# Performance work log

Measured on AMD Instinct MI355X. Metric: run time of the kernel, lower is better.

## Reference

```python
import jax, jax.numpy as jnp
import numpy as np

B, L, C, N = 64, 512, 1, 128  # batch, max seq len, num_conjugates, num_tags


def setup_inputs() -> dict:
    key = jax.random.key(0)
    k1, k2, k3, k4, k5 = jax.random.split(key, 5)
    emissions = jax.random.normal(k1, (B, L, C, N), dtype=jnp.float32)
    transitions = jax.random.normal(k2, (C, N, N), dtype=jnp.float32) * 0.01
    start_transitions = jax.random.normal(k3, (C, N), dtype=jnp.float32) * 0.01
    end_transitions = jax.random.normal(k4, (C, N), dtype=jnp.float32) * 0.01
    lengths = jax.random.randint(k5, (B,), 1, L + 1)  # valid lengths in [1, L]
    return {
        "emissions": emissions,
        "transitions": transitions,
        "start_transitions": start_transitions,
        "end_transitions": end_transitions,
        "lengths": lengths,
    }


def reference(emissions, transitions, start_transitions, end_transitions, lengths):
    # CRF log-partition (forward algorithm in the log semiring).
    # emissions: [B, L, C, N]; transitions: [C, N, N]; start/end: [C, N]; lengths: [B]
    b, l, c, n = emissions.shape
    # alpha_0 = start + emission at t=0  -> [B, C, N]
    alpha0 = start_transitions[None, :, :] + emissions[:, 0]

    e_rest = jnp.moveaxis(emissions[:, 1:], 1, 0)  # [L-1, B, C, N]
    t_idx = jnp.arange(1, l)

    def step(alpha, inp):
        e_t, t = inp
        # log-semiring mat-vec: logsumexp over previous tag axis
        scores = alpha[..., :, None] + transitions[None] + e_t[..., None, :]  # [B,C,N,N]
        new_alpha = jax.nn.logsumexp(scores, axis=2)  # [B, C, N]
        active = (t < lengths)[:, None, None]  # ragged mask: freeze finished sequences
        return jnp.where(active, new_alpha, alpha), None

    alpha, _ = jax.lax.scan(step, alpha0, (e_rest, t_idx))
    # terminate with end transitions -> log partition per (batch, conjugate)
    return jax.nn.logsumexp(alpha + end_transitions[None, :, :], axis=-1)  # [B, C]
```

## Files before the change

### kernel.cpp

```cpp
#include <hip/hip_runtime.h>


#define LOG2E 1.4426950408889634f
#define LN2   0.6931471805599453f

#define LDS_BARRIER() asm volatile("s_waitcnt lgkmcnt(0)\n\ts_barrier" ::: "memory")

typedef float    f2 __attribute__((ext_vector_type(2)));
typedef _Float16 h2 __attribute__((ext_vector_type(2)));

#define PKRTZ(a, b) __builtin_bit_cast(h2, __builtin_amdgcn_cvt_pkrtz((a), (b)))

template <int CTRL>
__device__ __forceinline__ float dpp_f(float x) {
    return __int_as_float(
        __builtin_amdgcn_mov_dpp(__float_as_int(x), CTRL, 0xF, 0xF, false));
}

__global__ __launch_bounds__(256)
__attribute__((amdgpu_waves_per_eu(1, 1)))
void crf_halves(
    const float* __restrict__ emissions,
    const float* __restrict__ transitions,
    const float* __restrict__ start_t,
    const float* __restrict__ end_t,
    const int*   __restrict__ lengths,
    float* __restrict__ wsV,
    int*   __restrict__ wsO)
{
    constexpr int N = 128;
    constexpr int L = 512;
    const int  bid = blockIdx.x;
    const bool isf = bid < 64;
    const int  b   = isf ? bid : bid - 64;
    const int  tid = threadIdx.x;
    const int  g   = tid >> 2;
    const int  k   = tid & 3;

    __shared__ alignas(16) float pbuf[2][80];

    h2 EA_0,  EA_1,  EA_2,  EA_3,  EA_4,  EA_5,  EA_6,  EA_7;
    h2 EA_8,  EA_9,  EA_10, EA_11, EA_12, EA_13, EA_14, EA_15;
    h2 EB_0,  EB_1,  EB_2,  EB_3,  EB_4,  EB_5,  EB_6,  EB_7;
    h2 EB_8,  EB_9,  EB_10, EB_11, EB_12, EB_13, EB_14, EB_15;
    if (isf) {
        const float* tb = transitions + (size_t)(32 * k) * N + 2 * g;
#define INIT_F(m)                                                              \
        {                                                                      \
            f2 r0 = *reinterpret_cast<const f2*>(tb + (size_t)(2 * (m)) * N);  \
            f2 r1 = *reinterpret_cast<const f2*>(tb + (size_t)(2 * (m) + 1) * N); \
            EA_##m = PKRTZ(__builtin_amdgcn_exp2f(r0.x * LOG2E),               \
                           __builtin_amdgcn_exp2f(r1.x * LOG2E));              \
            EB_##m = PKRTZ(__builtin_amdgcn_exp2f(r0.y * LOG2E),               \
                           __builtin_amdgcn_exp2f(r1.y * LOG2E));              \
        }
        INIT_F(0)  INIT_F(1)  INIT_F(2)  INIT_F(3)
        INIT_F(4)  INIT_F(5)  INIT_F(6)  INIT_F(7)
        INIT_F(8)  INIT_F(9)  INIT_F(10) INIT_F(11)
        INIT_F(12) INIT_F(13) INIT_F(14) INIT_F(15)
#undef INIT_F
    } else {
        const float* ra_ = transitions + (size_t)(2 * g) * N + 32 * k;
        const float* rb_ = transitions + (size_t)(2 * g + 1) * N + 32 * k;
#define INIT_B(m)                                                              \
        {                                                                      \
            f2 r0 = *reinterpret_cast<const f2*>(ra_ + 2 * (m));               \
            f2 r1 = *reinterpret_cast<const f2*>(rb_ + 2 * (m));               \
            EA_##m = PKRTZ(__builtin_amdgcn_exp2f(r0.x * LOG2E),               \
                           __builtin_amdgcn_exp2f(r0.y * LOG2E));              \
            EB_##m = PKRTZ(__builtin_amdgcn_exp2f(r1.x * LOG2E),               \
                           __builtin_amdgcn_exp2f(r1.y * LOG2E));              \
        }
        INIT_B(0)  INIT_B(1)  INIT_B(2)  INIT_B(3)
        INIT_B(4)  INIT_B(5)  INIT_B(6)  INIT_B(7)
        INIT_B(8)  INIT_B(9)  INIT_B(10) INIT_B(11)
        INIT_B(12) INIT_B(13) INIT_B(14) INIT_B(15)
#undef INIT_B
    }

    const int len = lengths[b];
    const int m   = (len - 1) >> 1;
    const float* eb = emissions + (size_t)b * L * N;

    int n_steps, e0, dstep; bool zfinal;
    if (isf) {
        n_steps = m; e0 = 1; dstep = 1; zfinal = false;
    } else {
        int total = len - 1 - m;
        n_steps = total > 0 ? total - 1 : 0;
        e0 = len - 2; if (e0 < 0) e0 = 0;
        dstep = -1;
        zfinal = total > 0;
    }

    int o = 0, cur = 0;
    float qA, qB;
    {
        const float* base = isf ? start_t : end_t;
        f2 bt = *reinterpret_cast<const f2*>(base + 2 * g);
        f2 ev;
        if (isf)         ev = *reinterpret_cast<const f2*>(eb + 2 * g);
        else if (zfinal) ev = *reinterpret_cast<const f2*>(eb + (size_t)(len - 1) * N + 2 * g);
        else           { ev.x = 0.f; ev.y = 0.f; }
        qA = __builtin_amdgcn_exp2f((bt.x + ev.x) * LOG2E);
        qB = __builtin_amdgcn_exp2f((bt.y + ev.y) * LOG2E);
        if (k == 0)
            pbuf[0][(g >> 4) * 20 + (g & 15)] =
                __builtin_bit_cast(float, PKRTZ(qA, qB));
    }
    LDS_BARRIER();

    auto eidx = [&](int n) {
        int nn = (n < n_steps) ? n : (n_steps - 1);
        if (nn < 0) nn = 0;
        return e0 + dstep * nn;
    };
    auto ldE = [&](int tt) {
        return *reinterpret_cast<const f2*>(eb + (size_t)tt * N + 2 * g);
    };

    auto STEP = [&](f2 ecur) {
        float q0w = pbuf[cur][0];
        const float4* pv = reinterpret_cast<const float4*>(&pbuf[cur][k * 20]);
        float4 Q0 = pv[0], Q1 = pv[1], Q2 = pv[2], Q3 = pv[3];

        unsigned u0 = __float_as_uint(q0w);
        int eS = (int)((u0 >> 10) & 0x1Fu) - 15;
        o += eS;
        float feS = (float)eS;
        float esA = __builtin_amdgcn_exp2f(ecur.x * LOG2E - feS);
        float esB = __builtin_amdgcn_exp2f(ecur.y * LOG2E - feS);

        float aA0 = 0.f, aA1 = 0.f, aB0 = 0.f, aB1 = 0.f;
#define D0(m_, Qc)                                                             \
        {                                                                      \
            h2 pm = __builtin_bit_cast(h2, Qc);                                \
            aA0 = __builtin_amdgcn_fdot2(pm, EA_##m_, aA0, false);             \
            aB0 = __builtin_amdgcn_fdot2(pm, EB_##m_, aB0, false);             \
        }
#define D1(m_, Qc)                                                             \
        {                                                                      \
            h2 pm = __builtin_bit_cast(h2, Qc);                                \
            aA1 = __builtin_amdgcn_fdot2(pm, EA_##m_, aA1, false);             \
            aB1 = __builtin_amdgcn_fdot2(pm, EB_##m_, aB1, false);             \
        }
        D0(0,  Q0.x) D1(1,  Q0.y) D0(2,  Q0.z) D1(3,  Q0.w)
        D0(4,  Q1.x) D1(5,  Q1.y) D0(6,  Q1.z) D1(7,  Q1.w)
        D0(8,  Q2.x) D1(9,  Q2.y) D0(10, Q2.z) D1(11, Q2.w)
        D0(12, Q3.x) D1(13, Q3.y) D0(14, Q3.z) D1(15, Q3.w)
#undef D0
#undef D1
        float dA = aA0 + aA1;
        float dB = aB0 + aB1;

        dA += dpp_f<0xB1>(dA); dB += dpp_f<0xB1>(dB);
        dA += dpp_f<0x4E>(dA); dB += dpp_f<0x4E>(dB);

        qA = esA * dA;
        qB = esB * dB;
        cur ^= 1;
        if (k == 0)
            pbuf[cur][(g >> 4) * 20 + (g & 15)] =
                __builtin_bit_cast(float, PKRTZ(qA, qB));
        LDS_BARRIER();
    };

    f2 ra = ldE(eidx(0));
    f2 rb = ldE(eidx(1));
    f2 rc = ldE(eidx(2));
    f2 rd = ldE(eidx(3));

    int n = 0;
    while (n < n_steps) {
        STEP(ra); ra = ldE(eidx(n + 4)); ++n; if (n >= n_steps) break;
        STEP(rb); rb = ldE(eidx(n + 4)); ++n; if (n >= n_steps) break;
        STEP(rc); rc = ldE(eidx(n + 4)); ++n; if (n >= n_steps) break;
        STEP(rd); rd = ldE(eidx(n + 4)); ++n;
    }
    if (zfinal) {
        f2 z; z.x = 0.f; z.y = 0.f;
        STEP(z);
    }

    float* wv = wsV + (size_t)((isf ? 0 : 64) + b) * 128;
    if (k == 0) {
        f2 q; q.x = qA; q.y = qB;
        *reinterpret_cast<f2*>(wv + 2 * g) = q;
    }
    if (tid == 0) wsO[(isf ? 0 : 64) + b] = o;
}

__global__ __launch_bounds__(64)
void crf_combine(const float* __restrict__ wsV, const int* __restrict__ wsO,
                 const int* __restrict__ lengths, float* __restrict__ out)
{
    const int b = blockIdx.x;
    const int g = threadIdx.x;
    f2 a = *reinterpret_cast<const f2*>(wsV + (size_t)b * 128 + 2 * g);
    f2 x = *reinterpret_cast<const f2*>(wsV + (size_t)(64 + b) * 128 + 2 * g);
    float v = a.x * x.x + a.y * x.y;
    #pragma unroll
    for (int s = 1; s < 64; s <<= 1) v += __shfl_xor(v, s);
    if (g == 0)
        out[b] = LN2 * ((float)(wsO[b] + wsO[64 + b]) +
                        __builtin_amdgcn_logf(v));
}

extern "C" void kernel_launch(void* const* d_in, const int* in_sizes, int n_in,
                              void* d_out, int out_size, void* d_ws, size_t ws_size,
                              hipStream_t stream) {
    const float* emissions   = (const float*)d_in[0];
    const float* transitions = (const float*)d_in[1];
    const float* start_t     = (const float*)d_in[2];
    const float* end_t       = (const float*)d_in[3];
    const int*   lengths     = (const int*)d_in[4];
    float* out = (float*)d_out;

    float* wsV = (float*)d_ws;
    int*   wsO = (int*)((char*)d_ws + 2 * 64 * 128 * sizeof(float));

    crf_halves<<<dim3(128), dim3(256), 0, stream>>>(
        emissions, transitions, start_t, end_t, lengths, wsV, wsO);
    crf_combine<<<dim3(64), dim3(64), 0, stream>>>(wsV, wsO, lengths, out);
}
```

Measured before the change: 131.5 us.

## Split CRF recurrence into four segments using MFMA matrix-product blocks for middle quarters

The sequence is now split into four quarters instead of two halves. The first and last quarters keep the forward and backward vector recurrences. The two middle quarters are computed by new blocks that build transfer-matrix products with 32x32x16 f16 MFMA instructions, using per-wave exponent rescaling. A reworked combine kernel multiplies the forward vector through both fp16 matrices and dots the result with the backward vector. This halves the serial dependency chain per block but adds matrix-matrix work, a 32 KB fp16 matrix write per block, and extra fp16 precision and scaling risk.

```diff
diff --git a/kernel.cpp b/kernel.cpp
--- a/kernel.cpp
+++ b/kernel.cpp
@@ -5,11 +5,17 @@
 #define LN2   0.6931471805599453f
 
 #define LDS_BARRIER() asm volatile("s_waitcnt lgkmcnt(0)\n\ts_barrier" ::: "memory")
-
-typedef float    f2 __attribute__((ext_vector_type(2)));
-typedef _Float16 h2 __attribute__((ext_vector_type(2)));
+#define LGKM0() asm volatile("s_waitcnt lgkmcnt(0)" ::: "memory")
+
+typedef float    f2  __attribute__((ext_vector_type(2)));
+typedef float    f4  __attribute__((ext_vector_type(4)));
+typedef float    f16f __attribute__((ext_vector_type(16)));
+typedef unsigned u4  __attribute__((ext_vector_type(4)));
+typedef _Float16 h2  __attribute__((ext_vector_type(2)));
+typedef _Float16 h8  __attribute__((ext_vector_type(8)));
 
 #define PKRTZ(a, b) __builtin_bit_cast(h2, __builtin_amdgcn_cvt_pkrtz((a), (b)))
+#define BITS(x)     __builtin_bit_cast(unsigned, (x))
 
 template <int CTRL>
 __device__ __forceinline__ float dpp_f(float x) {
@@ -19,191 +25,352 @@
 
 __global__ __launch_bounds__(256)
 __attribute__((amdgpu_waves_per_eu(1, 1)))
-void crf_halves(
+void crf_fused(
     const float* __restrict__ emissions,
     const float* __restrict__ transitions,
     const float* __restrict__ start_t,
     const float* __restrict__ end_t,
     const int*   __restrict__ lengths,
     float* __restrict__ wsV,
-    int*   __restrict__ wsO)
+    int*   __restrict__ wsO,
+    int*   __restrict__ wsMo,
+    _Float16* __restrict__ wsMh)
 {
     constexpr int N = 128;
     constexpr int L = 512;
-    const int  bid = blockIdx.x;
-    const bool isf = bid < 64;
-    const int  b   = isf ? bid : bid - 64;
-    const int  tid = threadIdx.x;
-    const int  g   = tid >> 2;
-    const int  k   = tid & 3;
+    const int bid  = blockIdx.x;
+    const int role = bid >> 6;
+    const int b    = bid & 63;
+    const int tid  = threadIdx.x;
+
+    const int len = lengths[b];
+    const int T   = len - 1;
+    const int qa  = T >> 2;
+    const int qb  = T >> 1;
+    const int qc  = (3 * T) >> 2;
+    const float* eb = emissions + (size_t)b * L * N;
 
     __shared__ alignas(16) float pbuf[2][80];
-
-    h2 EA_0,  EA_1,  EA_2,  EA_3,  EA_4,  EA_5,  EA_6,  EA_7;
-    h2 EA_8,  EA_9,  EA_10, EA_11, EA_12, EA_13, EA_14, EA_15;
-    h2 EB_0,  EB_1,  EB_2,  EB_3,  EB_4,  EB_5,  EB_6,  EB_7;
-    h2 EB_8,  EB_9,  EB_10, EB_11, EB_12, EB_13, EB_14, EB_15;
-    if (isf) {
-        const float* tb = transitions + (size_t)(32 * k) * N + 2 * g;
+    __shared__ alignas(16) float sbuf[4][128];
+
+    if (role < 2) {
+        const bool isf = (role == 0);
+        const int  g   = tid >> 2;
+        const int  k   = tid & 3;
+
+        h2 EA_0,  EA_1,  EA_2,  EA_3,  EA_4,  EA_5,  EA_6,  EA_7;
+        h2 EA_8,  EA_9,  EA_10, EA_11, EA_12, EA_13, EA_14, EA_15;
+        h2 EB_0,  EB_1,  EB_2,  EB_3,  EB_4,  EB_5,  EB_6,  EB_7;
+        h2 EB_8,  EB_9,  EB_10, EB_11, EB_12, EB_13, EB_14, EB_15;
+        if (isf) {
+            const float* tb = transitions + (size_t)(32 * k) * N + 2 * g;
 #define INIT_F(m)                                                              \
-        {                                                                      \
-            f2 r0 = *reinterpret_cast<const f2*>(tb + (size_t)(2 * (m)) * N);  \
-            f2 r1 = *reinterpret_cast<const f2*>(tb + (size_t)(2 * (m) + 1) * N); \
-            EA_##m = PKRTZ(__builtin_amdgcn_exp2f(r0.x * LOG2E),               \
-                           __builtin_amdgcn_exp2f(r1.x * LOG2E));              \
-            EB_##m = PKRTZ(__builtin_amdgcn_exp2f(r0.y * LOG2E),               \
-                           __builtin_amdgcn_exp2f(r1.y * LOG2E));              \
-        }
-        INIT_F(0)  INIT_F(1)  INIT_F(2)  INIT_F(3)
-        INIT_F(4)  INIT_F(5)  INIT_F(6)  INIT_F(7)
-        INIT_F(8)  INIT_F(9)  INIT_F(10) INIT_F(11)
-        INIT_F(12) INIT_F(13) INIT_F(14) INIT_F(15)
+            {                                                                  \
+                f2 r0 = *reinterpret_cast<const f2*>(tb + (size_t)(2 * (m)) * N); \
+                f2 r1 = *reinterpret_cast<const f2*>(tb + (size_t)(2 * (m) + 1) * N); \
+                EA_##m = PKRTZ(__builtin_amdgcn_exp2f(r0.x * LOG2E),           \
+                               __builtin_amdgcn_exp2f(r1.x * LOG2E));          \
+                EB_##m = PKRTZ(__builtin_amdgcn_exp2f(r0.y * LOG2E),           \
+                               __builtin_amdgcn_exp2f(r1.y * LOG2E));          \
+            }
+            INIT_F(0)  INIT_F(1)  INIT_F(2)  INIT_F(3)
+            INIT_F(4)  INIT_F(5)  INIT_F(6)  INIT_F(7)
+            INIT_F(8)  INIT_F(9)  INIT_F(10) INIT_F(11)
+            INIT_F(12) INIT_F(13) INIT_F(14) INIT_F(15)
 #undef INIT_F
-    } else {
-        const float* ra_ = transitions + (size_t)(2 * g) * N + 32 * k;
-        const float* rb_ = transitions + (size_t)(2 * g + 1) * N + 32 * k;
+        } else {
+            const float* ra_ = transitions + (size_t)(2 * g) * N + 32 * k;
+            const float* rb_ = transitions + (size_t)(2 * g + 1) * N + 32 * k;
 #define INIT_B(m)                                                              \
-        {                                                                      \
-            f2 r0 = *reinterpret_cast<const f2*>(ra_ + 2 * (m));               \
-            f2 r1 = *reinterpret_cast<const f2*>(rb_ + 2 * (m));               \
-            EA_##m = PKRTZ(__builtin_amdgcn_exp2f(r0.x * LOG2E),               \
-                           __builtin_amdgcn_exp2f(r0.y * LOG2E));              \
-            EB_##m = PKRTZ(__builtin_amdgcn_exp2f(r1.x * LOG2E),               \
-                           __builtin_amdgcn_exp2f(r1.y * LOG2E));              \
-        }
-        INIT_B(0)  INIT_B(1)  INIT_B(2)  INIT_B(3)
-        INIT_B(4)  INIT_B(5)  INIT_B(6)  INIT_B(7)
-        INIT_B(8)  INIT_B(9)  INIT_B(10) INIT_B(11)
-        INIT_B(12) INIT_B(13) INIT_B(14) INIT_B(15)
+            {                                                                  \
+                f2 r0 = *reinterpret_cast<const f2*>(ra_ + 2 * (m));           \
+                f2 r1 = *reinterpret_cast<const f2*>(rb_ + 2 * (m));           \
+                EA_##m = PKRTZ(__builtin_amdgcn_exp2f(r0.x * LOG2E),           \
+                               __builtin_amdgcn_exp2f(r0.y * LOG2E));          \
+                EB_##m = PKRTZ(__builtin_amdgcn_exp2f(r1.x * LOG2E),           \
+                               __builtin_amdgcn_exp2f(r1.y * LOG2E));          \
+            }
+            INIT_B(0)  INIT_B(1)  INIT_B(2)  INIT_B(3)
+            INIT_B(4)  INIT_B(5)  INIT_B(6)  INIT_B(7)
+            INIT_B(8)  INIT_B(9)  INIT_B(10) INIT_B(11)
+            INIT_B(12) INIT_B(13) INIT_B(14) INIT_B(15)
 #undef INIT_B
-    }
-
-    const int len = lengths[b];
-    const int m   = (len - 1) >> 1;
-    const float* eb = emissions + (size_t)b * L * N;
-
-    int n_steps, e0, dstep; bool zfinal;
-    if (isf) {
-        n_steps = m; e0 = 1; dstep = 1; zfinal = false;
-    } else {
-        int total = len - 1 - m;
-        n_steps = total > 0 ? total - 1 : 0;
-        e0 = len - 2; if (e0 < 0) e0 = 0;
-        dstep = -1;
-        zfinal = total > 0;
-    }
-
-    int o = 0, cur = 0;
-    float qA, qB;
-    {
-        const float* base = isf ? start_t : end_t;
-        f2 bt = *reinterpret_cast<const f2*>(base + 2 * g);
-        f2 ev;
-        if (isf)         ev = *reinterpret_cast<const f2*>(eb + 2 * g);
-        else if (zfinal) ev = *reinterpret_cast<const f2*>(eb + (size_t)(len - 1) * N + 2 * g);
-        else           { ev.x = 0.f; ev.y = 0.f; }
-        qA = __builtin_amdgcn_exp2f((bt.x + ev.x) * LOG2E);
-        qB = __builtin_amdgcn_exp2f((bt.y + ev.y) * LOG2E);
-        if (k == 0)
-            pbuf[0][(g >> 4) * 20 + (g & 15)] =
-                __builtin_bit_cast(float, PKRTZ(qA, qB));
-    }
-    LDS_BARRIER();
-
-    auto eidx = [&](int n) {
-        int nn = (n < n_steps) ? n : (n_steps - 1);
-        if (nn < 0) nn = 0;
-        return e0 + dstep * nn;
-    };
-    auto ldE = [&](int tt) {
-        return *reinterpret_cast<const f2*>(eb + (size_t)tt * N + 2 * g);
-    };
-
-    auto STEP = [&](f2 ecur) {
-        float q0w = pbuf[cur][0];
-        const float4* pv = reinterpret_cast<const float4*>(&pbuf[cur][k * 20]);
-        float4 Q0 = pv[0], Q1 = pv[1], Q2 = pv[2], Q3 = pv[3];
-
-        unsigned u0 = __float_as_uint(q0w);
-        int eS = (int)((u0 >> 10) & 0x1Fu) - 15;
-        o += eS;
-        float feS = (float)eS;
-        float esA = __builtin_amdgcn_exp2f(ecur.x * LOG2E - feS);
-        float esB = __builtin_amdgcn_exp2f(ecur.y * LOG2E - feS);
-
-        float aA0 = 0.f, aA1 = 0.f, aB0 = 0.f, aB1 = 0.f;
-#define D0(m_, Qc)                                                             \
-        {                                                                      \
-            h2 pm = __builtin_bit_cast(h2, Qc);                                \
-            aA0 = __builtin_amdgcn_fdot2(pm, EA_##m_, aA0, false);             \
-            aB0 = __builtin_amdgcn_fdot2(pm, EB_##m_, aB0, false);             \
-        }
-#define D1(m_, Qc)                                                             \
-        {                                                                      \
-            h2 pm = __builtin_bit_cast(h2, Qc);                                \
-            aA1 = __builtin_amdgcn_fdot2(pm, EA_##m_, aA1, false);             \
-            aB1 = __builtin_amdgcn_fdot2(pm, EB_##m_, aB1, false);             \
-        }
-        D0(0,  Q0.x) D1(1,  Q0.y) D0(2,  Q0.z) D1(3,  Q0.w)
-        D0(4,  Q1.x) D1(5,  Q1.y) D0(6,  Q1.z) D1(7,  Q1.w)
-        D0(8,  Q2.x) D1(9,  Q2.y) D0(10, Q2.z) D1(11, Q2.w)
-        D0(12, Q3.x) D1(13, Q3.y) D0(14, Q3.z) D1(15, Q3.w)
+        }
+
+        int n_steps, e0, dstep; bool zfinal;
+        if (isf) {
+            n_steps = qa; e0 = 1; dstep = 1; zfinal = false;
+        } else {
+            int total = T - qc;
+            n_steps = total > 0 ? total - 1 : 0;
+            e0 = len - 2; if (e0 < 0) e0 = 0;
+            dstep = -1;
+            zfinal = total > 0;
+        }
+
+        int o = 0, cur = 0;
+        float qA, qB;
+        {
+            const float* base = isf ? start_t : end_t;
+            f2 bt = *reinterpret_cast<const f2*>(base + 2 * g);
+            f2 ev;
+            if (isf)         ev = *reinterpret_cast<const f2*>(eb + 2 * g);
+            else if (zfinal) ev = *reinterpret_cast<const f2*>(eb + (size_t)(len - 1) * N + 2 * g);
+            else           { ev.x = 0.f; ev.y = 0.f; }
+            qA = __builtin_amdgcn_exp2f((bt.x + ev.x) * LOG2E);
+            qB = __builtin_amdgcn_exp2f((bt.y + ev.y) * LOG2E);
+            if (k == 0)
+                pbuf[0][(g >> 4) * 20 + (g & 15)] =
+                    __builtin_bit_cast(float, PKRTZ(qA, qB));
+        }
+        LDS_BARRIER();
+
+        auto eidx = [&](int n) {
+            int nn = (n < n_steps) ? n : (n_steps - 1);
+            if (nn < 0) nn = 0;
+            return e0 + dstep * nn;
+        };
+        auto ldE = [&](int tt) {
+            return *reinterpret_cast<const f2*>(eb + (size_t)tt * N + 2 * g);
+        };
+
+        auto STEP = [&](f2 ecur) {
+            float q0w = pbuf[cur][0];
+            const float4* pv = reinterpret_cast<const float4*>(&pbuf[cur][k * 20]);
+            float4 Qa = pv[0], Qb = pv[1], Qc = pv[2], Qd = pv[3];
+
+            unsigned u0 = __float_as_uint(q0w);
+            int eS = (int)((u0 >> 10) & 0x1Fu) - 15;
+            o += eS;
+            float feS = (float)eS;
+            float esA = __builtin_amdgcn_exp2f(ecur.x * LOG2E - feS);
+            float esB = __builtin_amdgcn_exp2f(ecur.y * LOG2E - feS);
+
+            float aA0 = 0.f, aA1 = 0.f, aB0 = 0.f, aB1 = 0.f;
+#define D0(m_, Qc_)                                                            \
+            {                                                                  \
+                h2 pm = __builtin_bit_cast(h2, Qc_);                           \
+                aA0 = __builtin_amdgcn_fdot2(pm, EA_##m_, aA0, false);         \
+                aB0 = __builtin_amdgcn_fdot2(pm, EB_##m_, aB0, false);         \
+            }
+#define D1(m_, Qc_)                                                            \
+            {                                                                  \
+                h2 pm = __builtin_bit_cast(h2, Qc_);                           \
+                aA1 = __builtin_amdgcn_fdot2(pm, EA_##m_, aA1, false);         \
+                aB1 = __builtin_amdgcn_fdot2(pm, EB_##m_, aB1, false);         \
+            }
+            D0(0,  Qa.x) D1(1,  Qa.y) D0(2,  Qa.z) D1(3,  Qa.w)
+            D0(4,  Qb.x) D1(5,  Qb.y) D0(6,  Qb.z) D1(7,  Qb.w)
+            D0(8,  Qc.x) D1(9,  Qc.y) D0(10, Qc.z) D1(11, Qc.w)
+            D0(12, Qd.x) D1(13, Qd.y) D0(14, Qd.z) D1(15, Qd.w)
 #undef D0
 #undef D1
-        float dA = aA0 + aA1;
-        float dB = aB0 + aB1;
-
-        dA += dpp_f<0xB1>(dA); dB += dpp_f<0xB1>(dB);
-        dA += dpp_f<0x4E>(dA); dB += dpp_f<0x4E>(dB);
-
-        qA = esA * dA;
-        qB = esB * dB;
-        cur ^= 1;
-        if (k == 0)
-            pbuf[cur][(g >> 4) * 20 + (g & 15)] =
-                __builtin_bit_cast(float, PKRTZ(qA, qB));
-        LDS_BARRIER();
-    };
-
-    f2 ra = ldE(eidx(0));
-    f2 rb = ldE(eidx(1));
-    f2 rc = ldE(eidx(2));
-    f2 rd = ldE(eidx(3));
-
-    int n = 0;
-    while (n < n_steps) {
-        STEP(ra); ra = ldE(eidx(n + 4)); ++n; if (n >= n_steps) break;
-        STEP(rb); rb = ldE(eidx(n + 4)); ++n; if (n >= n_steps) break;
-        STEP(rc); rc = ldE(eidx(n + 4)); ++n; if (n >= n_steps) break;
-        STEP(rd); rd = ldE(eidx(n + 4)); ++n;
+            float dA = aA0 + aA1;
+            float dB = aB0 + aB1;
+            dA += dpp_f<0xB1>(dA); dB += dpp_f<0xB1>(dB);
+            dA += dpp_f<0x4E>(dA); dB += dpp_f<0x4E>(dB);
+
+            qA = esA * dA;
+            qB = esB * dB;
+            cur ^= 1;
+            if (k == 0)
+                pbuf[cur][(g >> 4) * 20 + (g & 15)] =
+                    __builtin_bit_cast(float, PKRTZ(qA, qB));
+            LDS_BARRIER();
+        };
+
+        f2 ra = ldE(eidx(0));
+        f2 rb = ldE(eidx(1));
+        f2 rc = ldE(eidx(2));
+        f2 rd = ldE(eidx(3));
+
+        int n = 0;
+        while (n < n_steps) {
+            STEP(ra); ra = ldE(eidx(n + 4)); ++n; if (n >= n_steps) break;
+            STEP(rb); rb = ldE(eidx(n + 4)); ++n; if (n >= n_steps) break;
+            STEP(rc); rc = ldE(eidx(n + 4)); ++n; if (n >= n_steps) break;
+            STEP(rd); rd = ldE(eidx(n + 4)); ++n;
+        }
+        if (zfinal) { f2 z; z.x = 0.f; z.y = 0.f; STEP(z); }
+
+        float* wv = wsV + (size_t)(role * 64 + b) * 128;
+        if (k == 0) {
+            f2 q; q.x = qA; q.y = qB;
+            *reinterpret_cast<f2*>(wv + 2 * g) = q;
+        }
+        if (tid == 0) wsO[role * 64 + b] = o;
+
+    } else {
+        const int w    = tid >> 6;
+        const int lidx = tid & 63;
+        const int h    = (tid >> 5) & 1;
+        const int nn   = tid & 31;
+        const int matid = role - 2;
+        const int tlo   = matid ? qb : qa;
+        const int nm    = matid ? (qc - qb) : (qb - qa);
+
+        h8 Afr[4][8];
+        #pragma unroll
+        for (int mt = 0; mt < 4; ++mt) {
+            #pragma unroll
+            for (int kb = 0; kb < 8; ++kb) {
+                u4 au;
+                #pragma unroll
+                for (int ep = 0; ep < 4; ++ep) {
+                    int ee0 = 2 * ep, ee1 = 2 * ep + 1;
+                    int k0 = 16 * kb + 4 * h + (ee0 & 3) + 8 * (ee0 >> 2);
+                    int k1 = 16 * kb + 4 * h + (ee1 & 3) + 8 * (ee1 >> 2);
+                    float v0 = __builtin_amdgcn_exp2f(
+                        transitions[k0 * N + 32 * mt + nn] * LOG2E);
+                    float v1 = __builtin_amdgcn_exp2f(
+                        transitions[k1 * N + 32 * mt + nn] * LOG2E);
+                    au[ep] = BITS(PKRTZ(v0, v1));
+                }
+                Afr[mt][kb] = __builtin_bit_cast(h8, au);
+            }
+        }
+
+        h8 B0[8], B1[8];
+        const int colg = 32 * w + nn;
+        #pragma unroll
+        for (int kb = 0; kb < 8; ++kb) {
+            u4 bu; bu[0] = 0u; bu[1] = 0u; bu[2] = 0u; bu[3] = 0u;
+            #pragma unroll
+            for (int e = 0; e < 8; ++e) {
+                int kk = 16 * kb + 4 * h + (e & 3) + 8 * (e >> 2);
+                if (kk == colg)
+                    bu[e >> 1] |= 0x3C00u << (16 * (e & 1));
+            }
+            B0[kb] = __builtin_bit_cast(h8, bu);
+        }
+        int o = 0;
+
+        auto ldEm = [&](int q) {
+            int qq = q; if (qq > nm - 1) qq = nm - 1; if (qq < 0) qq = 0;
+            int t = tlo + 1 + qq;
+            return *reinterpret_cast<const f2*>(eb + (size_t)t * N + 2 * lidx);
+        };
+
+        auto STEPm = [&](h8 (&Bs)[8], h8 (&Bd)[8], f2 ev) {
+            f2 sp;
+            sp.x = __builtin_amdgcn_exp2f(ev.x * LOG2E);
+            sp.y = __builtin_amdgcn_exp2f(ev.y * LOG2E);
+            *reinterpret_cast<f2*>(&sbuf[w][2 * lidx]) = sp;
+            LGKM0();
+
+            float sc = 1.0f;
+            #pragma unroll
+            for (int mt = 0; mt < 4; ++mt) {
+                f4 s0 = *reinterpret_cast<const f4*>(&sbuf[w][32 * mt + 4 * h]);
+                f4 s1 = *reinterpret_cast<const f4*>(&sbuf[w][32 * mt + 8 + 4 * h]);
+                f4 s2 = *reinterpret_cast<const f4*>(&sbuf[w][32 * mt + 16 + 4 * h]);
+                f4 s3 = *reinterpret_cast<const f4*>(&sbuf[w][32 * mt + 24 + 4 * h]);
+                f16f D = {0.f,0.f,0.f,0.f,0.f,0.f,0.f,0.f,
+                          0.f,0.f,0.f,0.f,0.f,0.f,0.f,0.f};
+                #pragma unroll
+                for (int kb = 0; kb < 8; ++kb)
+                    D = __builtin_amdgcn_mfma_f32_32x32x16_f16(
+                        Afr[mt][kb], Bs[kb], D, 0, 0, 0);
+                if (mt == 0) {
+                    int rb_ = __builtin_amdgcn_readfirstlane(__float_as_int(D[0]));
+                    int ex = (int)(((unsigned)rb_ >> 23) & 255u) - 127;
+                    if (ex > 24) ex = 24; if (ex < -24) ex = -24;
+                    o += ex;
+                    sc = __int_as_float((unsigned)(127 - ex) << 23);
+                }
+                u4 lo, hi;
+                lo[0] = BITS(PKRTZ(D[0]  * s0.x * sc, D[1]  * s0.y * sc));
+                lo[1] = BITS(PKRTZ(D[2]  * s0.z * sc, D[3]  * s0.w * sc));
+                lo[2] = BITS(PKRTZ(D[4]  * s1.x * sc, D[5]  * s1.y * sc));
+                lo[3] = BITS(PKRTZ(D[6]  * s1.z * sc, D[7]  * s1.w * sc));
+                hi[0] = BITS(PKRTZ(D[8]  * s2.x * sc, D[9]  * s2.y * sc));
+                hi[1] = BITS(PKRTZ(D[10] * s2.z * sc, D[11] * s2.w * sc));
+                hi[2] = BITS(PKRTZ(D[12] * s3.x * sc, D[13] * s3.y * sc));
+                hi[3] = BITS(PKRTZ(D[14] * s3.z * sc, D[15] * s3.w * sc));
+                Bd[2 * mt]     = __builtin_bit_cast(h8, lo);
+                Bd[2 * mt + 1] = __builtin_bit_cast(h8, hi);
+            }
+        };
+
+        f2 ra = ldEm(0), rb = ldEm(1);
+        int q = 0;
+        while (q + 1 < nm) {
+            STEPm(B0, B1, ra); ra = ldEm(q + 2);
+            STEPm(B1, B0, rb); rb = ldEm(q + 3);
+            q += 2;
+        }
+        if (q < nm) {
+            STEPm(B0, B1, ra);
+            #pragma unroll
+            for (int kb = 0; kb < 8; ++kb) B0[kb] = B1[kb];
+        }
+
+        _Float16* wm = wsMh + ((size_t)(matid * 64 + b) * 128 + (32 * w + nn)) * 128;
+        #pragma unroll
+        for (int kb = 0; kb < 8; ++kb) {
+            u4 bu = __builtin_bit_cast(u4, B0[kb]);
+            #pragma unroll
+            for (int e = 0; e < 8; ++e) {
+                int j = 16 * kb + 4 * h + (e & 3) + 8 * (e >> 2);
+                unsigned dw = bu[e >> 1];
+                unsigned short us = (unsigned short)((e & 1) ? (dw >> 16)
+                                                             : (dw & 0xFFFFu));
+                wm[j] = __builtin_bit_cast(_Float16, us);
+            }
+        }
+        if (lidx == 0) wsMo[(matid * 64 + b) * 4 + w] = o;
     }
-    if (zfinal) {
-        f2 z; z.x = 0.f; z.y = 0.f;
-        STEP(z);
-    }
-
-    float* wv = wsV + (size_t)((isf ? 0 : 64) + b) * 128;
-    if (k == 0) {
-        f2 q; q.x = qA; q.y = qB;
-        *reinterpret_cast<f2*>(wv + 2 * g) = q;
-    }
-    if (tid == 0) wsO[(isf ? 0 : 64) + b] = o;
 }
 
-__global__ __launch_bounds__(64)
+__global__ __launch_bounds__(128)
 void crf_combine(const float* __restrict__ wsV, const int* __restrict__ wsO,
-                 const int* __restrict__ lengths, float* __restrict__ out)
+                 const int* __restrict__ wsMo, const _Float16* __restrict__ wsMh,
+                 float* __restrict__ out)
 {
     const int b = blockIdx.x;
-    const int g = threadIdx.x;
-    f2 a = *reinterpret_cast<const f2*>(wsV + (size_t)b * 128 + 2 * g);
-    f2 x = *reinterpret_cast<const f2*>(wsV + (size_t)(64 + b) * 128 + 2 * g);
-    float v = a.x * x.x + a.y * x.y;
+    const int j = threadIdx.x;
+    __shared__ float stage[128];
+    __shared__ float redw[2];
+
+    int o10 = wsMo[(0 * 64 + b) * 4 + 0], o11 = wsMo[(0 * 64 + b) * 4 + 1];
+    int o12 = wsMo[(0 * 64 + b) * 4 + 2], o13 = wsMo[(0 * 64 + b) * 4 + 3];
+    int o20 = wsMo[(1 * 64 + b) * 4 + 0], o21 = wsMo[(1 * 64 + b) * 4 + 1];
+    int o22 = wsMo[(1 * 64 + b) * 4 + 2], o23 = wsMo[(1 * 64 + b) * 4 + 3];
+    int O1 = max(max(o10, o11), max(o12, o13));
+    int O2 = max(max(o20, o21), max(o22, o23));
+
+    float al = wsV[(size_t)(0 * 64 + b) * 128 + j];
+    int r1 = wsMo[(0 * 64 + b) * 4 + (j >> 5)];
+    stage[j] = al * __builtin_amdgcn_exp2f((float)(r1 - O1));
+    __syncthreads();
+
+    float v1 = 0.f;
+    const _Float16* M1 = wsMh + (size_t)(0 * 64 + b) * 128 * 128;
+    #pragma unroll 8
+    for (int i = 0; i < 128; ++i)
+        v1 += stage[i] * (float)M1[(size_t)i * 128 + j];
+    __syncthreads();
+
+    int r2 = wsMo[(1 * 64 + b) * 4 + (j >> 5)];
+    stage[j] = v1 * __builtin_amdgcn_exp2f((float)(r2 - O2));
+    __syncthreads();
+
+    float v2 = 0.f;
+    const _Float16* M2 = wsMh + (size_t)(1 * 64 + b) * 128 * 128;
+    #pragma unroll 8
+    for (int i = 0; i < 128; ++i)
+        v2 += stage[i] * (float)M2[(size_t)i * 128 + j];
+
+    float term = v2 * wsV[(size_t)(1 * 64 + b) * 128 + j];
     #pragma unroll
-    for (int s = 1; s < 64; s <<= 1) v += __shfl_xor(v, s);
-    if (g == 0)
-        out[b] = LN2 * ((float)(wsO[b] + wsO[64 + b]) +
-                        __builtin_amdgcn_logf(v));
+    for (int s = 1; s < 64; s <<= 1) term += __shfl_xor(term, s);
+    if ((j & 63) == 0) redw[j >> 6] = term;
+    __syncthreads();
+    if (j == 0) {
+        float V = redw[0] + redw[1];
+        out[b] = LN2 * ((float)(wsO[b] + wsO[64 + b] + O1 + O2) +
+                        __builtin_amdgcn_logf(V));
+    }
 }
 
 extern "C" void kernel_launch(void* const* d_in, const int* in_sizes, int n_in,
@@ -216,10 +383,12 @@
     const int*   lengths     = (const int*)d_in[4];
     float* out = (float*)d_out;
 
-    float* wsV = (float*)d_ws;
-    int*   wsO = (int*)((char*)d_ws + 2 * 64 * 128 * sizeof(float));
-
-    crf_halves<<<dim3(128), dim3(256), 0, stream>>>(
-        emissions, transitions, start_t, end_t, lengths, wsV, wsO);
-    crf_combine<<<dim3(64), dim3(64), 0, stream>>>(wsV, wsO, lengths, out);
+    float*    wsV  = (float*)d_ws;
+    int*      wsO  = (int*)((char*)d_ws + 65536);
+    int*      wsMo = (int*)((char*)d_ws + 66048);
+    _Float16* wsMh = (_Float16*)((char*)d_ws + 68096);
+
+    crf_fused<<<dim3(256), dim3(256), 0, stream>>>(
+        emissions, transitions, start_t, end_t, lengths, wsV, wsO, wsMo, wsMh);
+    crf_combine<<<dim3(64), dim3(128), 0, stream>>>(wsV, wsO, wsMo, wsMh, out);
 }
```

Result: slower. 184.9 us (+40.7%).
